# Kernel tuning notes

Hardware: AMD Instinct MI355X
Metric: run time of the kernel (lower is better)

Reference implementation:

```python
import jax, jax.numpy as jnp
import numpy as np

N = 8192      # nodes
IN_FEATS = 128
OUT_FEATS = 64
DEG = 16      # avg degree for random edges
NEG_SLOPE = 0.01  # nn.LeakyReLU default


def setup_inputs() -> dict:
    key = jax.random.key(0)
    k1, k2, k3, k4, k5, k6 = jax.random.split(key, 6)
    inputs = jax.random.normal(k1, (N, IN_FEATS), dtype=jnp.float32)
    # Random symmetric adjacency with self-loops (dense, as in the original module)
    us = jax.random.randint(k2, (N * DEG,), 0, N)
    vs = jax.random.randint(k3, (N * DEG,), 0, N)
    A = jnp.zeros((N, N), dtype=jnp.float32)
    A = A.at[us, vs].set(1.0)
    A = A.at[vs, us].set(1.0)
    idx = jnp.arange(N)
    A = A.at[idx, idx].set(1.0)
    # Linear layer params (torch nn.Linear: weight [out, in])
    W = jax.random.normal(k4, (OUT_FEATS, IN_FEATS), dtype=jnp.float32) * (1.0 / np.sqrt(IN_FEATS))
    b = jnp.zeros((OUT_FEATS,), dtype=jnp.float32)
    # attention params, torch.rand -> uniform [0,1)
    a1 = jax.random.uniform(k5, (1, OUT_FEATS), dtype=jnp.float32)
    a2 = jax.random.uniform(k6, (1, OUT_FEATS), dtype=jnp.float32)
    return {"inputs": inputs, "A": A, "W": W, "b": b, "a1": a1, "a2": a2}


def reference(inputs, A, W, b, a1, a2):
    z = inputs @ W.T + b                                  # [N, out]
    zi = jnp.sum(a1 * z, axis=1, keepdims=True)           # [N, 1]
    zj = jnp.sum(a2 * z, axis=1, keepdims=True)           # [N, 1]
    n = A.shape[0]
    idx = jnp.arange(n)
    diagA = jnp.diagonal(A)                               # A_ii
    # attention_A + attention_B = A*zi + diag(A_ii * zj)  (A*(eye*zj) only keeps diagonal)
    att = A * zi
    att = att.at[idx, idx].add(diagA * zj[:, 0])
    att = jax.nn.leaky_relu(att, NEG_SLOPE)
    att = jnp.exp(att) * A
    att = att / jnp.sum(att, axis=1, keepdims=True)       # row-normalize
    h = z - att @ z
    return jax.nn.relu(h)
```

## Files before the change

kernel.cpp:

```cpp
#include <hip/hip_runtime.h>
#include <math.h>

#define NN 8192
#define IN_F 128
#define OUT_F 64
#define NEG_SLOPE 0.01f
#define K1_ROWS 8
#define CAP 256

typedef int v4i __attribute__((ext_vector_type(4)));

__global__ __launch_bounds__(256, 4) void k1_linear(
    const float* __restrict__ X, const float* __restrict__ W,
    const float* __restrict__ b, const float* __restrict__ a1,
    const float* __restrict__ a2, float* __restrict__ z,
    float* __restrict__ ev, float* __restrict__ dv, int* __restrict__ degG)
{
    __shared__ float Wl[OUT_F * 129];
    __shared__ float xs[K1_ROWS * IN_F];
    const int t = threadIdx.x;
    const int blk = blockIdx.x;

    const int gid = blk * 256 + t;
    if (gid < NN) degG[gid] = 0;

    for (int idx = t; idx < OUT_F * IN_F; idx += 256) {
        int f = idx >> 7, k = idx & 127;
        Wl[f * 129 + k] = W[idx];
    }
    {
        const float4* Xv = reinterpret_cast<const float4*>(X + (size_t)blk * (K1_ROWS * IN_F));
        float4* xsv = reinterpret_cast<float4*>(xs);
        if (t < K1_ROWS * IN_F / 4) xsv[t] = Xv[t];
    }
    __syncthreads();

    const int wid = t >> 6;
    const int lane = t & 63;
    const float bias = b[lane];
    const float a1f = a1[lane], a2f = a2[lane];

#pragma unroll
    for (int r2 = 0; r2 < 2; ++r2) {
        const int row = wid * 2 + r2;
        float acc = 0.f;
#pragma unroll 8
        for (int k = 0; k < IN_F; ++k)
            acc = fmaf(xs[row * IN_F + k], Wl[lane * 129 + k], acc);
        const float zval = acc + bias;
        const int i = blk * K1_ROWS + row;
        z[i * OUT_F + lane] = zval;

        float p1 = a1f * zval;
        float p2 = a2f * zval;
#pragma unroll
        for (int off = 32; off > 0; off >>= 1) {
            p1 += __shfl_down(p1, off, 64);
            p2 += __shfl_down(p2, off, 64);
        }
        if (lane == 0) {
            const float s1 = p1;
            const float s2 = p1 + p2;
            const float l1 = s1 > 0.f ? s1 : NEG_SLOPE * s1;
            const float l2 = s2 > 0.f ? s2 : NEG_SLOPE * s2;
            ev[i] = expf(l1);
            dv[i] = expf(l2);
        }
    }
}

__global__ __launch_bounds__(256, 8) void k2a_sym(
    const float* __restrict__ A, int* __restrict__ degG, int* __restrict__ nbrG)
{
    const int i = blockIdx.x;
    const int t = threadIdx.x;
    const v4i* __restrict__ Arow = reinterpret_cast<const v4i*>(A + (size_t)i * NN);
    const int s0 = i >> 2;

#define APPEND(J)                                                             \
    {                                                                         \
        int k = atomicAdd(&degG[i], 1);                                       \
        if (k < CAP) nbrG[(size_t)i * CAP + k] = (J);                         \
        if ((J) > i) {                                                        \
            int k2 = atomicAdd(&degG[(J)], 1);                                \
            if (k2 < CAP) nbrG[(size_t)(J) * CAP + k2] = i;                    \
        }                                                                     \
    }

    int s = s0 + t;
    v4i cur = {0, 0, 0, 0};
    if (s < NN / 4) cur = Arow[s];

    while (s < NN / 4) {
        const int sn = s + 256;
        v4i nxt = {0, 0, 0, 0};
        if (sn < NN / 4) nxt = Arow[sn];
        if (((cur.x | cur.y) | (cur.z | cur.w)) != 0) {
            const int j0 = s * 4;
            if (cur.x != 0 && j0 + 0 >= i) APPEND(j0 + 0)
            if (cur.y != 0 && j0 + 1 >= i) APPEND(j0 + 1)
            if (cur.z != 0 && j0 + 2 >= i) APPEND(j0 + 2)
            if (cur.w != 0 && j0 + 3 >= i) APPEND(j0 + 3)
        }
        cur = nxt; s = sn;
    }
#undef APPEND
}

__global__ __launch_bounds__(256, 8) void k2b_gather(
    const int* __restrict__ degG, const int* __restrict__ nbrG,
    const float* __restrict__ z, const float* __restrict__ ev,
    const float* __restrict__ dv, float* __restrict__ out)
{
    const int t = threadIdx.x;
    const int wid = t >> 6, lane = t & 63;
    const int i = blockIdx.x * 4 + wid;

    const int cnt0 = degG[i];
    const int cnt = cnt0 < CAP ? cnt0 : CAP;
    const int* rowl = nbrG + (size_t)i * CAP;

    float acc = 0.f;
    for (int k0 = 0; k0 < cnt; k0 += 64) {
        const int m = (cnt - k0) < 64 ? (cnt - k0) : 64;
        const int jv = (lane < m) ? rowl[k0 + lane] : 0;
        int kk = 0;
        for (; kk + 4 <= m; kk += 4) {
            const int j0 = __shfl(jv, kk + 0, 64);
            const int j1 = __shfl(jv, kk + 1, 64);
            const int j2 = __shfl(jv, kk + 2, 64);
            const int j3 = __shfl(jv, kk + 3, 64);
            const float z0 = z[(size_t)j0 * OUT_F + lane];
            const float z1 = z[(size_t)j1 * OUT_F + lane];
            const float z2 = z[(size_t)j2 * OUT_F + lane];
            const float z3 = z[(size_t)j3 * OUT_F + lane];
            acc += (z0 + z1) + (z2 + z3);
        }
        for (; kk < m; ++kk) {
            const int j = __shfl(jv, kk, 64);
            acc += z[(size_t)j * OUT_F + lane];
        }
    }

    const float degT = (float)cnt0;
    const float e = ev[i], d = dv[i];
    const float S = (degT - 1.f) * e + d;
    const float zif = z[(size_t)i * OUT_F + lane];
    const float h = zif * (1.f + (e - d) / S) - (e / S) * acc;
    out[(size_t)i * OUT_F + lane] = h > 0.f ? h : 0.f;
}

extern "C" void kernel_launch(void* const* d_in, const int* in_sizes, int n_in,
                              void* d_out, int out_size, void* d_ws, size_t ws_size,
                              hipStream_t stream) {
    const float* X  = (const float*)d_in[0];
    const float* A  = (const float*)d_in[1];
    const float* W  = (const float*)d_in[2];
    const float* b  = (const float*)d_in[3];
    const float* a1 = (const float*)d_in[4];
    const float* a2 = (const float*)d_in[5];
    float* out = (float*)d_out;

    char* ws = (char*)d_ws;
    float* z    = (float*)ws;
    float* ev   = (float*)(ws + (size_t)NN * OUT_F * 4);
    float* dv   = ev + NN;
    int*   degG = (int*)(dv + NN);
    int*   nbrG = degG + NN;

    k1_linear<<<NN / K1_ROWS, 256, 0, stream>>>(X, W, b, a1, a2, z, ev, dv, degG);
    k2a_sym<<<NN, 256, 0, stream>>>(A, degG, nbrG);
    k2b_gather<<<NN / 4, 256, 0, stream>>>(degG, nbrG, z, ev, dv, out);
}
```

Baseline: 61.53 us.

## Merge linear and adjacency-scan kernels into one heterogeneous launch

Fuses the linear projection and the adjacency symmetrization scan into a single grid, where the first 1024 blocks compute z, ev and dv and the rest scan rows of A. The aim is to run the small GEMM alongside the bandwidth-bound A scan and remove one kernel boundary. The linear part now reads X and W directly from global memory as float4 instead of staging them in LDS, and degree zeroing moves into a separate tiny kernel. The trade-off is an extra launch and more global/L2 traffic for W in the linear blocks.

```diff
diff --git a/kernel.cpp b/kernel.cpp
--- a/kernel.cpp
+++ b/kernel.cpp
@@ -5,75 +5,69 @@
 #define IN_F 128
 #define OUT_F 64
 #define NEG_SLOPE 0.01f
-#define K1_ROWS 8
+#define NLIN 1024
 #define CAP 256
 
 typedef int v4i __attribute__((ext_vector_type(4)));
 
-__global__ __launch_bounds__(256, 4) void k1_linear(
-    const float* __restrict__ X, const float* __restrict__ W,
-    const float* __restrict__ b, const float* __restrict__ a1,
-    const float* __restrict__ a2, float* __restrict__ z,
-    float* __restrict__ ev, float* __restrict__ dv, int* __restrict__ degG)
+__global__ void zero_deg(int* __restrict__ degG) {
+    const int g = blockIdx.x * 256 + threadIdx.x;
+    if (g < NN) degG[g] = 0;
+}
+
+__global__ __launch_bounds__(256, 8) void mega(
+    const float* __restrict__ A, const float* __restrict__ X,
+    const float* __restrict__ W, const float* __restrict__ b,
+    const float* __restrict__ a1, const float* __restrict__ a2,
+    float* __restrict__ z, float* __restrict__ ev, float* __restrict__ dv,
+    int* __restrict__ degG, int* __restrict__ nbrG)
 {
-    __shared__ float Wl[OUT_F * 129];
-    __shared__ float xs[K1_ROWS * IN_F];
     const int t = threadIdx.x;
-    const int blk = blockIdx.x;
 
-    const int gid = blk * 256 + t;
-    if (gid < NN) degG[gid] = 0;
-
-    for (int idx = t; idx < OUT_F * IN_F; idx += 256) {
-        int f = idx >> 7, k = idx & 127;
-        Wl[f * 129 + k] = W[idx];
-    }
-    {
-        const float4* Xv = reinterpret_cast<const float4*>(X + (size_t)blk * (K1_ROWS * IN_F));
-        float4* xsv = reinterpret_cast<float4*>(xs);
-        if (t < K1_ROWS * IN_F / 4) xsv[t] = Xv[t];
-    }
-    __syncthreads();
-
-    const int wid = t >> 6;
-    const int lane = t & 63;
-    const float bias = b[lane];
-    const float a1f = a1[lane], a2f = a2[lane];
+    if (blockIdx.x < NLIN) {
+        const int blk = blockIdx.x;
+        const int wid = t >> 6, lane = t & 63;
+        const float bias = b[lane];
+        const float a1f = a1[lane], a2f = a2[lane];
+        const float4* wr4 = reinterpret_cast<const float4*>(W + (size_t)lane * IN_F);
 
 #pragma unroll
-    for (int r2 = 0; r2 < 2; ++r2) {
-        const int row = wid * 2 + r2;
-        float acc = 0.f;
+        for (int r2 = 0; r2 < 2; ++r2) {
+            const int i = blk * 8 + wid * 2 + r2;
+            const float4* xr4 = reinterpret_cast<const float4*>(X + (size_t)i * IN_F);
+            float acc = 0.f;
 #pragma unroll 8
-        for (int k = 0; k < IN_F; ++k)
-            acc = fmaf(xs[row * IN_F + k], Wl[lane * 129 + k], acc);
-        const float zval = acc + bias;
-        const int i = blk * K1_ROWS + row;
-        z[i * OUT_F + lane] = zval;
+            for (int q = 0; q < IN_F / 4; ++q) {
+                const float4 xv = xr4[q];
+                const float4 wv = wr4[q];
+                acc = fmaf(xv.x, wv.x, acc);
+                acc = fmaf(xv.y, wv.y, acc);
+                acc = fmaf(xv.z, wv.z, acc);
+                acc = fmaf(xv.w, wv.w, acc);
+            }
+            const float zval = acc + bias;
+            z[(size_t)i * OUT_F + lane] = zval;
 
-        float p1 = a1f * zval;
-        float p2 = a2f * zval;
+            float p1 = a1f * zval;
+            float p2 = a2f * zval;
 #pragma unroll
-        for (int off = 32; off > 0; off >>= 1) {
-            p1 += __shfl_down(p1, off, 64);
-            p2 += __shfl_down(p2, off, 64);
+            for (int off = 32; off > 0; off >>= 1) {
+                p1 += __shfl_down(p1, off, 64);
+                p2 += __shfl_down(p2, off, 64);
+            }
+            if (lane == 0) {
+                const float s1 = p1;
+                const float s2 = p1 + p2;
+                const float l1 = s1 > 0.f ? s1 : NEG_SLOPE * s1;
+                const float l2 = s2 > 0.f ? s2 : NEG_SLOPE * s2;
+                ev[i] = expf(l1);
+                dv[i] = expf(l2);
+            }
         }
-        if (lane == 0) {
-            const float s1 = p1;
-            const float s2 = p1 + p2;
-            const float l1 = s1 > 0.f ? s1 : NEG_SLOPE * s1;
-            const float l2 = s2 > 0.f ? s2 : NEG_SLOPE * s2;
-            ev[i] = expf(l1);
-            dv[i] = expf(l2);
-        }
+        return;
     }
-}
 
-__global__ __launch_bounds__(256, 8) void k2a_sym(
-    const float* __restrict__ A, int* __restrict__ degG, int* __restrict__ nbrG)
-{
-    const int i = blockIdx.x;
-    const int t = threadIdx.x;
+    const int i = blockIdx.x - NLIN;
     const v4i* __restrict__ Arow = reinterpret_cast<const v4i*>(A + (size_t)i * NN);
     const int s0 = i >> 2;
 
@@ -83,7 +77,7 @@
         if (k < CAP) nbrG[(size_t)i * CAP + k] = (J);                         \
         if ((J) > i) {                                                        \
             int k2 = atomicAdd(&degG[(J)], 1);                                \
-            if (k2 < CAP) nbrG[(size_t)(J) * CAP + k2] = i;                    \
+            if (k2 < CAP) nbrG[(size_t)(J) * CAP + k2] = i;                   \
         }                                                                     \
     }
 
@@ -168,7 +162,7 @@
     int*   degG = (int*)(dv + NN);
     int*   nbrG = degG + NN;
 
-    k1_linear<<<NN / K1_ROWS, 256, 0, stream>>>(X, W, b, a1, a2, z, ev, dv, degG);
-    k2a_sym<<<NN, 256, 0, stream>>>(A, degG, nbrG);
+    zero_deg<<<NN / 256, 256, 0, stream>>>(degG);
+    mega<<<NLIN + NN, 256, 0, stream>>>(A, X, W, b, a1, a2, z, ev, dv, degG, nbrG);
     k2b_gather<<<NN / 4, 256, 0, stream>>>(degG, nbrG, z, ev, dv, out);
 }
```

New measurement: 83.40 us. +35.5%, slower.
